# Performance work log

Measured on AMD Instinct MI355X. Metric: run time of the kernel, lower is better.

## Reference

```python
import jax, jax.numpy as jnp
import numpy as np

N, D, H, O, E, K = 16384, 512, 512, 64, 8, 2


def _layernorm(x, g, b, eps=1e-5):
    mu = jnp.mean(x, axis=-1, keepdims=True)
    var = jnp.var(x, axis=-1, keepdims=True)
    return (x - mu) * jax.lax.rsqrt(var + eps) * g + b


def _gelu(x):
    return jax.nn.gelu(x, approximate=False)  # torch nn.GELU default (erf)


def setup_inputs() -> dict:
    key = jax.random.key(0)
    ks = jax.random.split(key, 20)
    s = 0.02
    return {
        "x": jax.random.normal(ks[0], (N, D), jnp.float32),
        # gate: Linear(D,H) -> LN(H) -> GELU -> Linear(H,E)
        "g_w1": jax.random.normal(ks[1], (D, H), jnp.float32) * s,
        "g_b1": jnp.zeros((H,), jnp.float32),
        "g_ln_g": jnp.ones((H,), jnp.float32),
        "g_ln_b": jnp.zeros((H,), jnp.float32),
        "g_w2": jax.random.normal(ks[2], (H, E), jnp.float32) * s,
        "g_b2": jnp.zeros((E,), jnp.float32),
        # experts (stacked over E): Linear(D,H)+LN+GELU, Linear(H,H)+LN+GELU, Linear(H,O)
        "e_w1": jax.random.normal(ks[3], (E, D, H), jnp.float32) * s,
        "e_b1": jnp.zeros((E, H), jnp.float32),
        "e_ln1_g": jnp.ones((E, H), jnp.float32),
        "e_ln1_b": jnp.zeros((E, H), jnp.float32),
        "e_w2": jax.random.normal(ks[4], (E, H, H), jnp.float32) * s,
        "e_b2": jnp.zeros((E, H), jnp.float32),
        "e_ln2_g": jnp.ones((E, H), jnp.float32),
        "e_ln2_b": jnp.zeros((E, H), jnp.float32),
        "e_w3": jax.random.normal(ks[5], (E, H, O), jnp.float32) * s,
        "e_b3": jnp.zeros((E, O), jnp.float32),
        # output projection Linear(O,O)
        "p_w": jax.random.normal(ks[6], (O, O), jnp.float32) * s,
        "p_b": jnp.zeros((O,), jnp.float32),
    }


def reference(x, g_w1, g_b1, g_ln_g, g_ln_b, g_w2, g_b2,
              e_w1, e_b1, e_ln1_g, e_ln1_b, e_w2, e_b2, e_ln2_g, e_ln2_b,
              e_w3, e_b3, p_w, p_b):
    n = x.shape[0]
    # --- gate ---
    gh = _gelu(_layernorm(x @ g_w1 + g_b1, g_ln_g, g_ln_b))
    gate_logits = gh @ g_w2 + g_b2                      # [N, E]
    gate_weights = jax.nn.softmax(gate_logits, axis=-1)
    top_k_weights, top_k_indices = jax.lax.top_k(gate_weights, K)
    top_k_weights = top_k_weights / jnp.sum(top_k_weights, axis=-1, keepdims=True)
    # dense per-token expert weights [N, E] (sum of top-k weights routed to each expert)
    w_dense = jnp.zeros((n, e_w1.shape[0]), x.dtype).at[
        jnp.arange(n)[:, None], top_k_indices].add(top_k_weights)
    # --- all experts on all tokens (faithful to dense loop) ---
    h1 = _gelu(_layernorm(jnp.einsum('nd,edh->enh', x, e_w1) + e_b1[:, None, :],
                          e_ln1_g[:, None, :], e_ln1_b[:, None, :]))
    h2 = _gelu(_layernorm(jnp.einsum('enh,ehk->enk', h1, e_w2) + e_b2[:, None, :],
                          e_ln2_g[:, None, :], e_ln2_b[:, None, :]))
    expert_out = jnp.einsum('enh,eho->eno', h2, e_w3) + e_b3[:, None, :]  # [E, N, O]
    combined = jnp.einsum('ne,eno->no', w_dense, expert_out)              # [N, O]
    output = combined @ p_w + p_b
    expert_usage = jnp.mean(gate_weights, axis=0)
    return (output, gate_weights, top_k_indices, top_k_weights, expert_usage)
```

## Files before the change

### kernel.cpp

```cpp
#include <hip/hip_runtime.h>
#include <hip/hip_bf16.h>

#define N_TOK 16384
#define MAX_SLOTS 34080
#define MAX_BLOCKS 216

typedef __attribute__((ext_vector_type(8))) short bf16x8;
typedef __attribute__((ext_vector_type(4))) float f32x4;
typedef unsigned short u16;

#define V_WAIT(N) asm volatile("s_waitcnt vmcnt(" #N ")" ::: "memory")
#define LGKM0()   asm volatile("s_waitcnt lgkmcnt(0)" ::: "memory")

__device__ __forceinline__ u16 f2bf(float f) {
  __hip_bfloat16 h = __float2bfloat16(f);
  union { __hip_bfloat16 b; u16 u; } c; c.b = h; return c.u;
}
__device__ __forceinline__ float bfbits2f(u16 u) {
  return __uint_as_float(((unsigned)u) << 16);
}
__device__ __forceinline__ float gelu_erf(float x) {
  return 0.5f * x * (1.0f + erff(x * 0.70710678118654752f));
}
__device__ __forceinline__ float gelu_fast(float x) {
  float u = x * (0.79788456f + 0.035677408f * x * x);
  float ex;
  asm("v_exp_f32 %0, %1" : "=v"(ex) : "v"(-2.8853901f * u));
  float den = 1.0f + ex;
  float r;
  asm("v_rcp_f32 %0, %1" : "=v"(r) : "v"(den));
  return x * r;
}
__device__ __forceinline__ void gload16(const u16* g, char* lds) {
  __builtin_amdgcn_global_load_lds(
      (const __attribute__((address_space(1))) void*)g,
      (__attribute__((address_space(3))) void*)lds, 16, 0, 0);
}

__global__ __launch_bounds__(256) void prep_x(const float* __restrict__ x,
                                              u16* __restrict__ xbf,
                                              u16* __restrict__ xlo) {
  size_t i = (size_t)blockIdx.x * 256 + threadIdx.x;
  float4 v = ((const float4*)x)[i];
  float a[4] = {v.x, v.y, v.z, v.w};
  union { u16 us[4]; unsigned long long ll; } hb, lb;
#pragma unroll
  for (int j = 0; j < 4; ++j) {
    u16 hu = f2bf(a[j]);
    hb.us[j] = hu;
    lb.us[j] = f2bf(a[j] - bfbits2f(hu));
  }
  *(unsigned long long*)(xbf + i * 4) = hb.ll;
  *(unsigned long long*)(xlo + i * 4) = lb.ll;
}

template <int C>
__global__ __launch_bounds__(256) void pack_w(const float* __restrict__ src,
                                              u16* __restrict__ dst, int R) {
  __shared__ float tl[64][65];
  const int e = blockIdx.z;
  const int k0 = blockIdx.x * 64, n0 = blockIdx.y * 64;
  const float* s = src + (size_t)e * R * C;
  const int tr = threadIdx.x >> 2;
  const int tc4 = (threadIdx.x & 3) * 16;
#pragma unroll
  for (int j = 0; j < 4; ++j) {
    float4 v = *(const float4*)(s + (size_t)(k0 + tr) * C + n0 + tc4 + j * 4);
    tl[tr][tc4 + j * 4 + 0] = v.x;
    tl[tr][tc4 + j * 4 + 1] = v.y;
    tl[tr][tc4 + j * 4 + 2] = v.z;
    tl[tr][tc4 + j * 4 + 3] = v.w;
  }
  __syncthreads();
  const int nl = threadIdx.x >> 2;
  const int kl = (threadIdx.x & 3) * 16;
  const int n = n0 + nl;
  const int sx = (n >> 1) & 3;
  const int t = (k0 + kl) >> 5;
  const int q0 = ((k0 + kl) & 31) >> 3;
#pragma unroll
  for (int c = 0; c < 2; ++c) {
    int q = q0 + c;
    int p = q ^ sx;
    union { u16 us[8]; unsigned long long ll[2]; } o;
#pragma unroll
    for (int j = 0; j < 8; ++j) o.us[j] = f2bf(tl[kl + c * 8 + j][nl]);
    u16* d = dst + (((size_t)e * (R / 32) + t) * C + n) * 32 + p * 8;
    ((unsigned long long*)d)[0] = o.ll[0];
    ((unsigned long long*)d)[1] = o.ll[1];
  }
}

__global__ __launch_bounds__(256) void prep_wcat(const float* __restrict__ gw1,
                                                 u16* __restrict__ wp) {
  int idx = blockIdx.x * 256 + threadIdx.x;
  int p = idx & 3;
  int n = (idx >> 2) & 511;
  int t = idx >> 11;
  int q = p ^ ((n >> 1) & 3);
  int k0 = t * 32 + q * 8;
  union { u16 us[8]; unsigned long long ll[2]; } o;
#pragma unroll
  for (int j = 0; j < 8; ++j) {
    int k = k0 + j;
    u16 v;
    if (k < 512) {
      v = f2bf(gw1[k * 512 + n]);
    } else if (k < 1024) {
      float w = gw1[(k - 512) * 512 + n];
      v = f2bf(w - bfbits2f(f2bf(w)));
    } else {
      v = f2bf(gw1[(k - 1024) * 512 + n]);
    }
    o.us[j] = v;
  }
  unsigned long long* d = (unsigned long long*)(wp + (size_t)idx * 8);
  d[0] = o.ll[0];
  d[1] = o.ll[1];
}

__global__ __launch_bounds__(256) void prep_w2t(const float* __restrict__ gw2,
                                                float* __restrict__ w2t) {
  int i = blockIdx.x * 256 + threadIdx.x;
  int e = i >> 9, k = i & 511;
  w2t[i] = gw2[k * 8 + e];
}

template <int FM, int ROUTED, int GATHER, int LNOUT, int FAST>
__global__ __launch_bounds__(512, 2) void gemm_core(
    const u16* __restrict__ A, const u16* __restrict__ A2,
    const u16* __restrict__ Wp, long w_estride, int klen, long osplit,
    const float* __restrict__ bias, int b_estride,
    const float* __restrict__ lng, const float* __restrict__ lnb,
    u16* __restrict__ outb, float* __restrict__ outf,
    const int* __restrict__ slot_token, const int* __restrict__ blk_e,
    const int* __restrict__ blk_tok0) {
  constexpr int BM = FM * 32;
  constexpr int AG = FM * 2;
  constexpr int ABYTES = BM * 64;
  constexpr int BUF = ABYTES + 32768;
  constexpr int NL = AG + 32;
  constexpr int L = (NL + 7) / 8;
  constexpr int TSU = 16384;
  extern __shared__ char smem[];

  const int tid = threadIdx.x;
  const int lane = tid & 63;
  const int wv = tid >> 6;
  const int wm = (wv & 1) * (FM * 16);
  const int wn = (wv >> 1) * 128;
  const int l15 = lane & 15;
  const int lk = lane >> 4;
  const int swzk16 = (lk ^ ((l15 >> 1) & 3)) << 4;

  int e, row0, kt0, kbase;
  if (ROUTED) {
    e = blk_e[blockIdx.x];
    if (e < 0) return;
    row0 = blk_tok0[blockIdx.x];
    kt0 = 0; kbase = 0;
  } else {
    e = 0;
    row0 = blockIdx.x * BM;
    kbase = blockIdx.y * klen;
    kt0 = kbase >> 5;
  }
  const u16* We = Wp + (size_t)e * w_estride;

  const int lrq = lane >> 2;
  const int cse = (((lane & 3) ^ ((lane >> 3) & 3)) << 3);
  size_t off[L];
  int ldsoff[L], typ[L];
#pragma unroll
  for (int i = 0; i < L; ++i) {
    int id = wv + 8 * i;
    if (id >= NL) { typ[i] = 2; off[i] = 0; ldsoff[i] = 0; continue; }
    if (id < AG) {
      int lr = id * 16 + lrq;
      long grow = GATHER ? (long)slot_token[row0 + lr] : (long)(row0 + lr);
      off[i] = (size_t)grow * 512 + cse;
      ldsoff[i] = id * 1024 + lane * 16;
      typ[i] = 0;
    } else {
      int bg = id - AG;
      off[i] = (size_t)bg * 512 + lane * 8;
      ldsoff[i] = ABYTES + bg * 1024 + lane * 16;
      typ[i] = 1;
    }
  }

  float bias_v[8], g_v[8], b_v[8];
  if constexpr (LNOUT) {
    const float* be = bias + (size_t)e * b_estride;
    const float* ge = lng + (size_t)e * b_estride;
    const float* bbe = lnb + (size_t)e * b_estride;
#pragma unroll
    for (int fn = 0; fn < 8; ++fn) {
      int col = wn + fn * 16 + l15;
      bias_v[fn] = be[col]; g_v[fn] = ge[col]; b_v[fn] = bbe[col];
    }
  }

  auto STAGE = [&](int t, char* b) {
    const int kg = kbase + t * 32;
    const u16* Aseg = A;
    int kc = kg;
    if (A2) {
      if (kg >= 1024) { Aseg = A2; kc = kg - 1024; }
      else if (kg >= 512) kc = kg - 512;
    }
    const u16* Bt = We + (size_t)(kt0 + t) * TSU;
#pragma unroll
    for (int i = 0; i < L; ++i) {
      if (typ[i] == 0)      gload16(Aseg + off[i] + kc, b + ldsoff[i]);
      else if (typ[i] == 1) gload16(Bt + off[i], b + ldsoff[i]);
    }
  };

  f32x4 acc[FM][8];
#pragma unroll
  for (int i = 0; i < FM; ++i)
#pragma unroll
    for (int j = 0; j < 8; ++j) acc[i][j] = (f32x4){0.f, 0.f, 0.f, 0.f};

  const int nt = klen / 32;

  V_WAIT(0);
  STAGE(0, smem);
  STAGE(1, smem + BUF);
  STAGE(2, smem + 2 * BUF);

  int bsel = 0;
  for (int t = 0; t < nt; ++t) {
    if constexpr (FM == 5) {
      if (t < nt - 2)       { if (wv < 2) V_WAIT(12); else V_WAIT(10); }
      else if (t == nt - 2) { if (wv < 2) V_WAIT(6);  else V_WAIT(5); }
      else                  V_WAIT(0);
    } else {
      if (t < nt - 2)       V_WAIT(10);
      else if (t == nt - 2) V_WAIT(5);
      else                  V_WAIT(0);
    }
    __builtin_amdgcn_s_barrier();
    char* cur = smem + bsel * BUF;
    char* cB = cur + ABYTES;
    bf16x8 af[FM];
#pragma unroll
    for (int fm = 0; fm < FM; ++fm)
      af[fm] = *(const bf16x8*)(cur + (wm + fm * 16 + l15) * 64 + swzk16);
#pragma unroll
    for (int fn = 0; fn < 8; ++fn) {
      bf16x8 bv = *(const bf16x8*)(cB + (wn + fn * 16 + l15) * 64 + swzk16);
#pragma unroll
      for (int fm = 0; fm < FM; ++fm)
        acc[fm][fn] = __builtin_amdgcn_mfma_f32_16x16x32_bf16(
            af[fm], bv, acc[fm][fn], 0, 0, 0);
    }
    LGKM0();
    __builtin_amdgcn_s_barrier();
    if (t + 3 < nt) STAGE(t + 3, cur);
    bsel = (bsel == 2) ? 0 : bsel + 1;
  }

  if constexpr (LNOUT) {
#pragma unroll
    for (int fm = 0; fm < FM; ++fm)
#pragma unroll
      for (int fn = 0; fn < 8; ++fn)
#pragma unroll
        for (int r = 0; r < 4; ++r) acc[fm][fn][r] += bias_v[fn];

    float* redS1 = (float*)smem;
    float* redS2 = redS1 + 4 * BM;
    const int g = wv >> 1;
#pragma unroll
    for (int fm = 0; fm < FM; ++fm)
#pragma unroll
      for (int r = 0; r < 4; ++r) {
        float a1 = 0.f, a2 = 0.f;
#pragma unroll
        for (int fn = 0; fn < 8; ++fn) {
          float v = acc[fm][fn][r];
          a1 += v; a2 += v * v;
        }
#pragma unroll
        for (int m = 1; m < 16; m <<= 1) {
          a1 += __shfl_xor(a1, m, 64);
          a2 += __shfl_xor(a2, m, 64);
        }
        if (l15 == 0) {
          int row = wm + fm * 16 + lk * 4 + r;
          redS1[g * BM + row] = a1;
          redS2[g * BM + row] = a2;
        }
      }
    __syncthreads();
#pragma unroll
    for (int fm = 0; fm < FM; ++fm)
#pragma unroll
      for (int r = 0; r < 4; ++r) {
        int row = wm + fm * 16 + lk * 4 + r;
        float S1 = 0.f, S2 = 0.f;
#pragma unroll
        for (int q = 0; q < 4; ++q) {
          S1 += redS1[q * BM + row];
          S2 += redS2[q * BM + row];
        }
        float mu = S1 * (1.0f / 512.0f);
        float var = S2 * (1.0f / 512.0f) - mu * mu;
        float rs = rsqrtf(var + 1e-5f);
        size_t rowg = (size_t)(row0 + row);
#pragma unroll
        for (int fn = 0; fn < 8; ++fn) {
          int col = wn + fn * 16 + l15;
          float v = (acc[fm][fn][r] - mu) * rs * g_v[fn] + b_v[fn];
          v = FAST ? gelu_fast(v) : gelu_erf(v);
          outb[rowg * 512 + col] = f2bf(v);
        }
      }
  } else {
    float* dst = outf + (size_t)blockIdx.y * osplit;
#pragma unroll
    for (int fm = 0; fm < FM; ++fm)
#pragma unroll
      for (int r = 0; r < 4; ++r) {
        size_t rowg = (size_t)(row0 + wm + fm * 16 + lk * 4 + r);
#pragma unroll
        for (int fn = 0; fn < 8; ++fn)
          dst[rowg * 512 + wn + fn * 16 + l15] = acc[fm][fn][r];
      }
  }
}

__global__ __launch_bounds__(256) void gate2_topk(
    const float* __restrict__ gh0, const float* __restrict__ gh1,
    const float* __restrict__ b1, const float* __restrict__ lng,
    const float* __restrict__ lnb, const float* __restrict__ w2t,
    const float* __restrict__ b2, float* __restrict__ gwout,
    float* __restrict__ idxout, float* __restrict__ tkwout) {
  const int lane = threadIdx.x & 63;
  const int wv = threadIdx.x >> 6;
  const int t = blockIdx.x * 4 + wv;
  const int c0 = lane * 8;
  float v[8];
  {
    float4 a0 = *(const float4*)(gh0 + (size_t)t * 512 + c0);
    float4 a1 = *(const float4*)(gh0 + (size_t)t * 512 + c0 + 4);
    float4 h0 = *(const float4*)(gh1 + (size_t)t * 512 + c0);
    float4 h1 = *(const float4*)(gh1 + (size_t)t * 512 + c0 + 4);
    float4 bb0 = *(const float4*)(b1 + c0);
    float4 bb1 = *(const float4*)(b1 + c0 + 4);
    v[0] = a0.x + h0.x + bb0.x; v[1] = a0.y + h0.y + bb0.y;
    v[2] = a0.z + h0.z + bb0.z; v[3] = a0.w + h0.w + bb0.w;
    v[4] = a1.x + h1.x + bb1.x; v[5] = a1.y + h1.y + bb1.y;
    v[6] = a1.z + h1.z + bb1.z; v[7] = a1.w + h1.w + bb1.w;
  }
  float s1 = 0.f, s2 = 0.f;
#pragma unroll
  for (int j = 0; j < 8; ++j) { s1 += v[j]; s2 += v[j] * v[j]; }
#pragma unroll
  for (int m = 1; m < 64; m <<= 1) {
    s1 += __shfl_xor(s1, m, 64);
    s2 += __shfl_xor(s2, m, 64);
  }
  float mu = s1 * (1.0f / 512.0f);
  float var = s2 * (1.0f / 512.0f) - mu * mu;
  float rs = rsqrtf(var + 1e-5f);
  float y[8];
  {
    float4 g0 = *(const float4*)(lng + c0);
    float4 g1 = *(const float4*)(lng + c0 + 4);
    float4 q0 = *(const float4*)(lnb + c0);
    float4 q1 = *(const float4*)(lnb + c0 + 4);
    float gg[8] = {g0.x, g0.y, g0.z, g0.w, g1.x, g1.y, g1.z, g1.w};
    float qq[8] = {q0.x, q0.y, q0.z, q0.w, q1.x, q1.y, q1.z, q1.w};
#pragma unroll
    for (int j = 0; j < 8; ++j)
      y[j] = gelu_erf((v[j] - mu) * rs * gg[j] + qq[j]);
  }
  float logit[8];
#pragma unroll
  for (int e = 0; e < 8; ++e) {
    const float4* wr = (const float4*)(w2t + e * 512 + c0);
    float4 w0 = wr[0], w1 = wr[1];
    float p = y[0] * w0.x + y[1] * w0.y + y[2] * w0.z + y[3] * w0.w +
              y[4] * w1.x + y[5] * w1.y + y[6] * w1.z + y[7] * w1.w;
#pragma unroll
    for (int m = 1; m < 64; m <<= 1) p += __shfl_xor(p, m, 64);
    logit[e] = p + b2[e];
  }
  if (lane == 0) {
    float mx = logit[0];
#pragma unroll
    for (int e = 1; e < 8; ++e) mx = fmaxf(mx, logit[e]);
    float w[8], ssum = 0.f;
#pragma unroll
    for (int e = 0; e < 8; ++e) { w[e] = expf(logit[e] - mx); ssum += w[e]; }
    float inv = 1.0f / ssum;
#pragma unroll
    for (int e = 0; e < 8; ++e) w[e] *= inv;
    float w1v = -1.f, w2v = -1.f; int i1 = 0, i2 = 0;
#pragma unroll
    for (int e = 0; e < 8; ++e) {
      float vv = w[e];
      if (vv > w1v)      { w2v = w1v; i2 = i1; w1v = vv; i1 = e; }
      else if (vv > w2v) { w2v = vv; i2 = e; }
    }
    float s = w1v + w2v;
#pragma unroll
    for (int e = 0; e < 8; ++e) gwout[t * 8 + e] = w[e];
    idxout[t * 2] = (float)i1; idxout[t * 2 + 1] = (float)i2;
    tkwout[t * 2] = w1v / s;   tkwout[t * 2 + 1] = w2v / s;
  }
}

__global__ __launch_bounds__(256) void usage_k(const float* __restrict__ gw,
                                               float* __restrict__ usage) {
  __shared__ float r[256];
  int e = blockIdx.x;
  float s = 0.f;
  for (int t = threadIdx.x; t < N_TOK; t += 256) s += gw[t * 8 + e];
  r[threadIdx.x] = s;
  __syncthreads();
  for (int st = 128; st > 0; st >>= 1) {
    if (threadIdx.x < st) r[threadIdx.x] += r[threadIdx.x + st];
    __syncthreads();
  }
  if (threadIdx.x == 0) usage[e] = r[0] * (1.0f / (float)N_TOK);
}

__global__ __launch_bounds__(256) void count_hist(const float* __restrict__ idxout,
                                                  int* __restrict__ blk_cnt) {
  __shared__ int h[8];
  if (threadIdx.x < 8) h[threadIdx.x] = 0;
  __syncthreads();
  int t = blockIdx.x * 256 + threadIdx.x;
  int e0 = (int)idxout[t * 2], e1 = (int)idxout[t * 2 + 1];
  atomicAdd(&h[e0], 1);
  atomicAdd(&h[e1], 1);
  __syncthreads();
  if (threadIdx.x < 8) blk_cnt[blockIdx.x * 8 + threadIdx.x] = h[threadIdx.x];
}

__global__ __launch_bounds__(512) void k_offsets2(
    const int* __restrict__ blk_cnt, int* __restrict__ sbase,
    int* __restrict__ blk_e, int* __restrict__ blk_tok0) {
  __shared__ int cnt[64][8];
  __shared__ int ecnt[8];
  __shared__ int offs[8];
  const int tid = threadIdx.x;
  cnt[tid >> 3][tid & 7] = blk_cnt[tid];
  __syncthreads();
  if (tid < 8) {
    int s = 0;
    for (int b = 0; b < 64; ++b) s += cnt[b][tid];
    ecnt[tid] = s;
  }
  __syncthreads();
  if (tid == 0) {
    int off = 0;
    for (int e = 0; e < 8; ++e) {
      offs[e] = off;
      off += ((ecnt[e] + 159) / 160) * 160;
    }
  }
  __syncthreads();
  {
    int b = tid >> 3, e = tid & 7;
    int s = offs[e];
    for (int bp = 0; bp < b; ++bp) s += cnt[bp][e];
    sbase[tid] = s;
  }
  for (int b = tid; b < MAX_BLOCKS; b += 512) {
    int acc = 0, be = -1, bt = 0;
#pragma unroll
    for (int e = 0; e < 8; ++e) {
      int nbe = (ecnt[e] + 159) / 160;
      if (b >= acc && b < acc + nbe) { be = e; bt = offs[e] + (b - acc) * 160; }
      acc += nbe;
    }
    blk_e[b] = be;
    blk_tok0[b] = bt;
  }
}

__global__ __launch_bounds__(256) void k_padinit(int* __restrict__ slot_token,
                                                 float* __restrict__ slot_w) {
  int i = blockIdx.x * 256 + threadIdx.x;
  if (i < MAX_SLOTS) { slot_token[i] = 0; slot_w[i] = 0.f; }
}

__global__ __launch_bounds__(256) void k_scatter2(
    const float* __restrict__ idxout, const float* __restrict__ tkwout,
    const int* __restrict__ sbase, int* __restrict__ slot_token,
    float* __restrict__ slot_w, int* __restrict__ tok_slot) {
  __shared__ int lpos[8];
  if (threadIdx.x < 8) lpos[threadIdx.x] = 0;
  __syncthreads();
  int t = blockIdx.x * 256 + threadIdx.x;
#pragma unroll
  for (int k = 0; k < 2; ++k) {
    int e = (int)idxout[t * 2 + k];
    int lr = atomicAdd(&lpos[e], 1);
    int s = sbase[blockIdx.x * 8 + e] + lr;
    slot_token[s] = t;
    slot_w[s] = tkwout[t * 2 + k];
    tok_slot[t * 2 + k] = s;
  }
}

__global__ __launch_bounds__(512) void gemm3_eo(
    const u16* __restrict__ h, const u16* __restrict__ w3p,
    const float* __restrict__ b3, const float* __restrict__ slot_w,
    const int* __restrict__ blk_e, const int* __restrict__ blk_tok0,
    float* __restrict__ eo) {
  constexpr int ABYTES = 10240;
  constexpr int BUF = ABYTES + 4096;
  __shared__ char smem[3 * BUF];
  int e = blk_e[blockIdx.x];
  if (e < 0) return;
  int row0 = blk_tok0[blockIdx.x];

  const int tid = threadIdx.x;
  const int lane = tid & 63;
  const int wv = tid >> 6;
  const int wm = (wv & 1) * 80;
  const int wn = (wv >> 1) * 16;
  const int l15 = lane & 15, lk = lane >> 4;
  const int swzk16 = (lk ^ ((l15 >> 1) & 3)) << 4;
  const u16* we = w3p + (size_t)e * 32768;

  const int lrq = lane >> 2;
  const int cse = (((lane & 3) ^ ((lane >> 3) & 3)) << 3);
  size_t off[2];
  int ldsoff[2], typ[2];
#pragma unroll
  for (int i = 0; i < 2; ++i) {
    int id = wv + 8 * i;
    if (id >= 14) { typ[i] = 2; off[i] = 0; ldsoff[i] = 0; continue; }
    if (id < 10) {
      off[i] = (size_t)(row0 + id * 16 + lrq) * 512 + cse;
      ldsoff[i] = id * 1024 + lane * 16;
      typ[i] = 0;
    } else {
      int bg = id - 10;
      off[i] = (size_t)bg * 512 + lane * 8;
      ldsoff[i] = ABYTES + bg * 1024 + lane * 16;
      typ[i] = 1;
    }
  }

  float b3v = b3[e * 64 + wn + l15];
  float swv[5];
#pragma unroll
  for (int fm = 0; fm < 5; ++fm)
    swv[fm] = slot_w[row0 + wm + fm * 16 + lk * 4];
  float swr[5][4];
#pragma unroll
  for (int fm = 0; fm < 5; ++fm)
#pragma unroll
    for (int r = 0; r < 4; ++r)
      swr[fm][r] = slot_w[row0 + wm + fm * 16 + lk * 4 + r];
  (void)swv;

  auto STAGE = [&](int t, char* b) {
#pragma unroll
    for (int i = 0; i < 2; ++i) {
      if (typ[i] == 0)      gload16(h + off[i] + t * 32, b + ldsoff[i]);
      else if (typ[i] == 1) gload16(we + (size_t)t * 2048 + off[i], b + ldsoff[i]);
    }
  };

  f32x4 acc[5];
#pragma unroll
  for (int j = 0; j < 5; ++j) acc[j] = (f32x4){0.f, 0.f, 0.f, 0.f};

  V_WAIT(0);
  STAGE(0, smem);
  STAGE(1, smem + BUF);
  STAGE(2, smem + 2 * BUF);

  int bsel = 0;
  for (int t = 0; t < 16; ++t) {
    if (t < 14)       { if (wv < 6) V_WAIT(4); else V_WAIT(2); }
    else if (t == 14) { if (wv < 6) V_WAIT(2); else V_WAIT(1); }
    else              V_WAIT(0);
    __builtin_amdgcn_s_barrier();
    char* cur = smem + bsel * BUF;
    char* cB = cur + ABYTES;
    bf16x8 bv = *(const bf16x8*)(cB + (wn + l15) * 64 + swzk16);
#pragma unroll
    for (int fm = 0; fm < 5; ++fm) {
      bf16x8 a = *(const bf16x8*)(cur + (wm + fm * 16 + l15) * 64 + swzk16);
      acc[fm] = __builtin_amdgcn_mfma_f32_16x16x32_bf16(a, bv, acc[fm], 0, 0, 0);
    }
    LGKM0();
    __builtin_amdgcn_s_barrier();
    if (t + 3 < 16) STAGE(t + 3, cur);
    bsel = (bsel == 2) ? 0 : bsel + 1;
  }

#pragma unroll
  for (int fm = 0; fm < 5; ++fm)
#pragma unroll
    for (int r = 0; r < 4; ++r) {
      int row = wm + fm * 16 + lk * 4 + r;
      eo[(size_t)(row0 + row) * 64 + wn + l15] = swr[fm][r] * (acc[fm][r] + b3v);
    }
}

__global__ __launch_bounds__(256) void combine_proj(
    const float* __restrict__ eo, const int* __restrict__ tok_slot,
    const float* __restrict__ pw, const float* __restrict__ pb,
    float* __restrict__ outp) {
  __shared__ float cs[64][68];
  __shared__ float pws[64][68];
  const int t0 = blockIdx.x * 64;
  const int tq = threadIdx.x & 3;
  const int tt = threadIdx.x >> 2;
#pragma unroll
  for (int j = 0; j < 4; ++j) {
    float4 v = *(const float4*)(pw + tt * 64 + tq * 16 + j * 4);
    *(float4*)&pws[tt][tq * 16 + j * 4] = v;
  }
  {
    int t = t0 + tt;
    int s1 = tok_slot[t * 2], s2 = tok_slot[t * 2 + 1];
#pragma unroll
    for (int j = 0; j < 4; ++j) {
      float4 a = *(const float4*)(eo + (size_t)s1 * 64 + tq * 16 + j * 4);
      float4 b = *(const float4*)(eo + (size_t)s2 * 64 + tq * 16 + j * 4);
      float4 c = {a.x + b.x, a.y + b.y, a.z + b.z, a.w + b.w};
      *(float4*)&cs[tt][tq * 16 + j * 4] = c;
    }
  }
  __syncthreads();
  float o[16];
#pragma unroll
  for (int i = 0; i < 16; ++i) o[i] = 0.f;
  for (int j = 0; j < 64; ++j) {
    float c = cs[tt][j];
#pragma unroll
    for (int q4 = 0; q4 < 4; ++q4) {
      float4 p = *(const float4*)&pws[j][tq * 16 + q4 * 4];
      o[q4 * 4 + 0] += c * p.x;
      o[q4 * 4 + 1] += c * p.y;
      o[q4 * 4 + 2] += c * p.z;
      o[q4 * 4 + 3] += c * p.w;
    }
  }
#pragma unroll
  for (int i = 0; i < 16; ++i)
    outp[(size_t)(t0 + tt) * 64 + tq * 16 + i] = o[i] + pb[tq * 16 + i];
}

extern "C" void kernel_launch(void* const* d_in, const int* in_sizes, int n_in,
                              void* d_out, int out_size, void* d_ws, size_t ws_size,
                              hipStream_t stream) {
  const float* x      = (const float*)d_in[0];
  const float* g_w1   = (const float*)d_in[1];
  const float* g_b1   = (const float*)d_in[2];
  const float* g_lng  = (const float*)d_in[3];
  const float* g_lnb  = (const float*)d_in[4];
  const float* g_w2   = (const float*)d_in[5];
  const float* g_b2   = (const float*)d_in[6];
  const float* e_w1   = (const float*)d_in[7];
  const float* e_b1   = (const float*)d_in[8];
  const float* e_ln1g = (const float*)d_in[9];
  const float* e_ln1b = (const float*)d_in[10];
  const float* e_w2   = (const float*)d_in[11];
  const float* e_b2   = (const float*)d_in[12];
  const float* e_ln2g = (const float*)d_in[13];
  const float* e_ln2b = (const float*)d_in[14];
  const float* e_w3   = (const float*)d_in[15];
  const float* e_b3   = (const float*)d_in[16];
  const float* p_w    = (const float*)d_in[17];
  const float* p_b    = (const float*)d_in[18];

  char* ws = (char*)d_ws;
  u16*   x_bf  = (u16*)(ws);
  u16*   x_lo  = (u16*)(ws + (16ull << 20));
  u16*   e_w1p = (u16*)(ws + (32ull << 20));
  u16*   e_w2p = (u16*)(ws + (36ull << 20));
  u16*   e_w3p = (u16*)(ws + (40ull << 20));
  u16*   wcat  = (u16*)(ws + (41ull << 20));
  float* w2t   = (float*)(ws + (43ull << 20));
  float* gh0   = (float*)(ws + (44ull << 20));
  float* gh1   = (float*)(ws + (76ull << 20));
  u16*   h     = (u16*)(ws + (44ull << 20));
  float* eo    = (float*)(ws + (112ull << 20));
  int*   slot_token = (int*)(ws + (121ull << 20));
  float* slot_w     = (float*)(ws + (121ull << 20) + (1ull << 18));
  int*   tok_slot   = (int*)(ws + (121ull << 20) + (2ull << 18));
  int*   blk_cnt    = (int*)(ws + (122ull << 20));
  int*   sbase      = blk_cnt + 512;
  int*   blk_e      = blk_cnt + 1024;
  int*   blk_tok0   = blk_cnt + 2048;
  if (ws_size < (123ull << 20)) return;

  float* fout = (float*)d_out;
  float* o_output = fout;
  float* o_gatew  = fout + 1048576;
  float* o_idx    = fout + 1179648;
  float* o_topw   = fout + 1212416;
  float* o_usage  = fout + 1245184;

  (void)hipFuncSetAttribute((const void*)gemm_core<4, 0, 0, 0, 0>,
                            hipFuncAttributeMaxDynamicSharedMemorySize, 122880);
  (void)hipFuncSetAttribute((const void*)gemm_core<5, 1, 1, 1, 1>,
                            hipFuncAttributeMaxDynamicSharedMemorySize, 129024);
  (void)hipFuncSetAttribute((const void*)gemm_core<5, 1, 0, 1, 1>,
                            hipFuncAttributeMaxDynamicSharedMemorySize, 129024);

  prep_x<<<8192, 256, 0, stream>>>(x, x_bf, x_lo);
  pack_w<512><<<dim3(8, 8, 8), 256, 0, stream>>>(e_w1, e_w1p, 512);
  pack_w<512><<<dim3(8, 8, 8), 256, 0, stream>>>(e_w2, e_w2p, 512);
  pack_w<64><<<dim3(8, 1, 8), 256, 0, stream>>>(e_w3, e_w3p, 512);
  prep_wcat<<<384, 256, 0, stream>>>(g_w1, wcat);
  prep_w2t<<<16, 256, 0, stream>>>(g_w2, w2t);

  gemm_core<4, 0, 0, 0, 0><<<dim3(N_TOK / 128, 2), 512, 122880, stream>>>(
      x_bf, x_lo, wcat, 0, 768, (long)N_TOK * 512, nullptr, 0,
      nullptr, nullptr, nullptr, gh0, nullptr, nullptr, nullptr);
  gate2_topk<<<N_TOK / 4, 256, 0, stream>>>(gh0, gh1, g_b1, g_lng, g_lnb,
                                            w2t, g_b2, o_gatew, o_idx, o_topw);
  usage_k<<<8, 256, 0, stream>>>(o_gatew, o_usage);

  count_hist<<<64, 256, 0, stream>>>(o_idx, blk_cnt);
  k_offsets2<<<1, 512, 0, stream>>>(blk_cnt, sbase, blk_e, blk_tok0);
  k_padinit<<<(MAX_SLOTS + 255) / 256, 256, 0, stream>>>(slot_token, slot_w);
  k_scatter2<<<64, 256, 0, stream>>>(o_idx, o_topw, sbase, slot_token, slot_w,
                                     tok_slot);

  gemm_core<5, 1, 1, 1, 1><<<MAX_BLOCKS, 512, 129024, stream>>>(
      x_bf, nullptr, e_w1p, 512 * 512, 512, 0, e_b1, 512,
      e_ln1g, e_ln1b, h, nullptr, slot_token, blk_e, blk_tok0);
  gemm_core<5, 1, 0, 1, 1><<<MAX_BLOCKS, 512, 129024, stream>>>(
      h, nullptr, e_w2p, 512 * 512, 512, 0, e_b2, 512,
      e_ln2g, e_ln2b, h, nullptr, slot_token, blk_e, blk_tok0);
  gemm3_eo<<<MAX_BLOCKS, 512, 0, stream>>>(h, e_w3p, e_b3, slot_w, blk_e,
                                           blk_tok0, eo);
  combine_proj<<<N_TOK / 64, 256, 0, stream>>>(eo, tok_slot, p_w, p_b, o_output);
}
```

Baseline: 212.5 us.

## Run expert GEMMs in FP8 with fp8 activations and packed fp8 weights

Converts the three routed expert GEMMs from bf16 to FP8 (e4m3) MFMA. The input x, the packed expert weights and the intermediate hidden activations are stored as fp8 with a new 64-byte K-tile layout. This halves the number of K-loop iterations and the bytes loaded per tile, targeting memory traffic and MFMA throughput in the expert stage. The gate GEMM stays bf16 and is split into its own specialized kernel. The trade-off is a substantial loss of precision in the expert outputs, which risks exceeding the accuracy tolerance.

```diff
diff --git a/kernel.cpp b/kernel.cpp
--- a/kernel.cpp
+++ b/kernel.cpp
@@ -8,6 +8,8 @@
 typedef __attribute__((ext_vector_type(8))) short bf16x8;
 typedef __attribute__((ext_vector_type(4))) float f32x4;
 typedef unsigned short u16;
+typedef unsigned char u8;
+typedef long i64;
 
 #define V_WAIT(N) asm volatile("s_waitcnt vmcnt(" #N ")" ::: "memory")
 #define LGKM0()   asm volatile("s_waitcnt lgkmcnt(0)" ::: "memory")
@@ -31,7 +33,10 @@
   asm("v_rcp_f32 %0, %1" : "=v"(r) : "v"(den));
   return x * r;
 }
-__device__ __forceinline__ void gload16(const u16* g, char* lds) {
+__device__ __forceinline__ u8 f2fp8(float f) {
+  return (u8)(__builtin_amdgcn_cvt_pk_fp8_f32(f, f, 0, false) & 0xff);
+}
+__device__ __forceinline__ void gload16(const void* g, char* lds) {
   __builtin_amdgcn_global_load_lds(
       (const __attribute__((address_space(1))) void*)g,
       (__attribute__((address_space(3))) void*)lds, 16, 0, 0);
@@ -39,7 +44,8 @@
 
 __global__ __launch_bounds__(256) void prep_x(const float* __restrict__ x,
                                               u16* __restrict__ xbf,
-                                              u16* __restrict__ xlo) {
+                                              u16* __restrict__ xlo,
+                                              u8* __restrict__ xf8) {
   size_t i = (size_t)blockIdx.x * 256 + threadIdx.x;
   float4 v = ((const float4*)x)[i];
   float a[4] = {v.x, v.y, v.z, v.w};
@@ -52,11 +58,14 @@
   }
   *(unsigned long long*)(xbf + i * 4) = hb.ll;
   *(unsigned long long*)(xlo + i * 4) = lb.ll;
+  int w8 = __builtin_amdgcn_cvt_pk_fp8_f32(a[0], a[1], 0, false);
+  w8 = __builtin_amdgcn_cvt_pk_fp8_f32(a[2], a[3], w8, true);
+  *(int*)(xf8 + i * 4) = w8;
 }
 
 template <int C>
-__global__ __launch_bounds__(256) void pack_w(const float* __restrict__ src,
-                                              u16* __restrict__ dst, int R) {
+__global__ __launch_bounds__(256) void pack_w_f8(const float* __restrict__ src,
+                                                 u8* __restrict__ dst, int R) {
   __shared__ float tl[64][65];
   const int e = blockIdx.z;
   const int k0 = blockIdx.x * 64, n0 = blockIdx.y * 64;
@@ -75,20 +84,22 @@
   const int nl = threadIdx.x >> 2;
   const int kl = (threadIdx.x & 3) * 16;
   const int n = n0 + nl;
-  const int sx = (n >> 1) & 3;
-  const int t = (k0 + kl) >> 5;
-  const int q0 = ((k0 + kl) & 31) >> 3;
-#pragma unroll
-  for (int c = 0; c < 2; ++c) {
-    int q = q0 + c;
-    int p = q ^ sx;
-    union { u16 us[8]; unsigned long long ll[2]; } o;
-#pragma unroll
-    for (int j = 0; j < 8; ++j) o.us[j] = f2bf(tl[kl + c * 8 + j][nl]);
-    u16* d = dst + (((size_t)e * (R / 32) + t) * C + n) * 32 + p * 8;
-    ((unsigned long long*)d)[0] = o.ll[0];
-    ((unsigned long long*)d)[1] = o.ll[1];
-  }
+  const int T = R / 64;
+  const int t = (k0 + kl) >> 6;
+  const int q = ((k0 + kl) >> 4) & 3;
+  const int p = q ^ ((n >> 1) & 3);
+  uint4 o;
+  unsigned w[4];
+#pragma unroll
+  for (int j = 0; j < 4; ++j) {
+    int ww = __builtin_amdgcn_cvt_pk_fp8_f32(tl[kl + 4 * j][nl],
+                                             tl[kl + 4 * j + 1][nl], 0, false);
+    ww = __builtin_amdgcn_cvt_pk_fp8_f32(tl[kl + 4 * j + 2][nl],
+                                         tl[kl + 4 * j + 3][nl], ww, true);
+    w[j] = (unsigned)ww;
+  }
+  o.x = w[0]; o.y = w[1]; o.z = w[2]; o.w = w[3];
+  *(uint4*)(dst + (((size_t)e * T + t) * C + n) * 64 + p * 16) = o;
 }
 
 __global__ __launch_bounds__(256) void prep_wcat(const float* __restrict__ gw1,
@@ -126,15 +137,11 @@
   w2t[i] = gw2[k * 8 + e];
 }
 
-template <int FM, int ROUTED, int GATHER, int LNOUT, int FAST>
-__global__ __launch_bounds__(512, 2) void gemm_core(
+template <int FM>
+__global__ __launch_bounds__(512, 2) void gemm_gate(
     const u16* __restrict__ A, const u16* __restrict__ A2,
-    const u16* __restrict__ Wp, long w_estride, int klen, long osplit,
-    const float* __restrict__ bias, int b_estride,
-    const float* __restrict__ lng, const float* __restrict__ lnb,
-    u16* __restrict__ outb, float* __restrict__ outf,
-    const int* __restrict__ slot_token, const int* __restrict__ blk_e,
-    const int* __restrict__ blk_tok0) {
+    const u16* __restrict__ Wp, int klen, long osplit,
+    float* __restrict__ outf) {
   constexpr int BM = FM * 32;
   constexpr int AG = FM * 2;
   constexpr int ABYTES = BM * 64;
@@ -153,19 +160,9 @@
   const int lk = lane >> 4;
   const int swzk16 = (lk ^ ((l15 >> 1) & 3)) << 4;
 
-  int e, row0, kt0, kbase;
-  if (ROUTED) {
-    e = blk_e[blockIdx.x];
-    if (e < 0) return;
-    row0 = blk_tok0[blockIdx.x];
-    kt0 = 0; kbase = 0;
-  } else {
-    e = 0;
-    row0 = blockIdx.x * BM;
-    kbase = blockIdx.y * klen;
-    kt0 = kbase >> 5;
-  }
-  const u16* We = Wp + (size_t)e * w_estride;
+  const int row0 = blockIdx.x * BM;
+  const int kbase = blockIdx.y * klen;
+  const int kt0 = kbase >> 5;
 
   const int lrq = lane >> 2;
   const int cse = (((lane & 3) ^ ((lane >> 3) & 3)) << 3);
@@ -176,9 +173,7 @@
     int id = wv + 8 * i;
     if (id >= NL) { typ[i] = 2; off[i] = 0; ldsoff[i] = 0; continue; }
     if (id < AG) {
-      int lr = id * 16 + lrq;
-      long grow = GATHER ? (long)slot_token[row0 + lr] : (long)(row0 + lr);
-      off[i] = (size_t)grow * 512 + cse;
+      off[i] = (size_t)(row0 + id * 16 + lrq) * 512 + cse;
       ldsoff[i] = id * 1024 + lane * 16;
       typ[i] = 0;
     } else {
@@ -189,27 +184,13 @@
     }
   }
 
-  float bias_v[8], g_v[8], b_v[8];
-  if constexpr (LNOUT) {
-    const float* be = bias + (size_t)e * b_estride;
-    const float* ge = lng + (size_t)e * b_estride;
-    const float* bbe = lnb + (size_t)e * b_estride;
-#pragma unroll
-    for (int fn = 0; fn < 8; ++fn) {
-      int col = wn + fn * 16 + l15;
-      bias_v[fn] = be[col]; g_v[fn] = ge[col]; b_v[fn] = bbe[col];
-    }
-  }
-
   auto STAGE = [&](int t, char* b) {
     const int kg = kbase + t * 32;
     const u16* Aseg = A;
     int kc = kg;
-    if (A2) {
-      if (kg >= 1024) { Aseg = A2; kc = kg - 1024; }
-      else if (kg >= 512) kc = kg - 512;
-    }
-    const u16* Bt = We + (size_t)(kt0 + t) * TSU;
+    if (kg >= 1024) { Aseg = A2; kc = kg - 1024; }
+    else if (kg >= 512) kc = kg - 512;
+    const u16* Bt = Wp + (size_t)(kt0 + t) * TSU;
 #pragma unroll
     for (int i = 0; i < L; ++i) {
       if (typ[i] == 0)      gload16(Aseg + off[i] + kc, b + ldsoff[i]);
@@ -224,7 +205,6 @@
     for (int j = 0; j < 8; ++j) acc[i][j] = (f32x4){0.f, 0.f, 0.f, 0.f};
 
   const int nt = klen / 32;
-
   V_WAIT(0);
   STAGE(0, smem);
   STAGE(1, smem + BUF);
@@ -232,15 +212,9 @@
 
   int bsel = 0;
   for (int t = 0; t < nt; ++t) {
-    if constexpr (FM == 5) {
-      if (t < nt - 2)       { if (wv < 2) V_WAIT(12); else V_WAIT(10); }
-      else if (t == nt - 2) { if (wv < 2) V_WAIT(6);  else V_WAIT(5); }
-      else                  V_WAIT(0);
-    } else {
-      if (t < nt - 2)       V_WAIT(10);
-      else if (t == nt - 2) V_WAIT(5);
-      else                  V_WAIT(0);
-    }
+    if (t < nt - 2)       V_WAIT(10);
+    else if (t == nt - 2) V_WAIT(5);
+    else                  V_WAIT(0);
     __builtin_amdgcn_s_barrier();
     char* cur = smem + bsel * BUF;
     char* cB = cur + ABYTES;
@@ -262,74 +236,185 @@
     bsel = (bsel == 2) ? 0 : bsel + 1;
   }
 
-  if constexpr (LNOUT) {
-#pragma unroll
-    for (int fm = 0; fm < FM; ++fm)
+  float* dst = outf + (size_t)blockIdx.y * osplit;
+#pragma unroll
+  for (int fm = 0; fm < FM; ++fm)
+#pragma unroll
+    for (int r = 0; r < 4; ++r) {
+      size_t rowg = (size_t)(row0 + wm + fm * 16 + lk * 4 + r);
 #pragma unroll
       for (int fn = 0; fn < 8; ++fn)
-#pragma unroll
-        for (int r = 0; r < 4; ++r) acc[fm][fn][r] += bias_v[fn];
-
-    float* redS1 = (float*)smem;
-    float* redS2 = redS1 + 4 * BM;
-    const int g = wv >> 1;
-#pragma unroll
-    for (int fm = 0; fm < FM; ++fm)
-#pragma unroll
-      for (int r = 0; r < 4; ++r) {
-        float a1 = 0.f, a2 = 0.f;
-#pragma unroll
-        for (int fn = 0; fn < 8; ++fn) {
-          float v = acc[fm][fn][r];
-          a1 += v; a2 += v * v;
-        }
-#pragma unroll
-        for (int m = 1; m < 16; m <<= 1) {
-          a1 += __shfl_xor(a1, m, 64);
-          a2 += __shfl_xor(a2, m, 64);
-        }
-        if (l15 == 0) {
-          int row = wm + fm * 16 + lk * 4 + r;
-          redS1[g * BM + row] = a1;
-          redS2[g * BM + row] = a2;
-        }
+        dst[rowg * 512 + wn + fn * 16 + l15] = acc[fm][fn][r];
+    }
+}
+
+template <int GATHER>
+__global__ __launch_bounds__(512, 2) void gemm_f8(
+    const u8* __restrict__ A, const u8* __restrict__ Wp, long w_estride,
+    const float* __restrict__ bias, const float* __restrict__ lng,
+    const float* __restrict__ lnb, u8* __restrict__ outb,
+    const int* __restrict__ slot_token, const int* __restrict__ blk_e,
+    const int* __restrict__ blk_tok0) {
+  constexpr int FM = 5, BM = 160, AG = 10;
+  constexpr int ABYTES = BM * 64;
+  constexpr int BUF = ABYTES + 32768;
+  constexpr int NL = AG + 32;
+  constexpr int L = 6;
+  extern __shared__ char smem[];
+
+  const int tid = threadIdx.x;
+  const int lane = tid & 63;
+  const int wv = tid >> 6;
+  const int wm = (wv & 1) * 80;
+  const int wn = (wv >> 1) * 128;
+  const int l15 = lane & 15;
+  const int lk = lane >> 4;
+  const int sx = (l15 >> 1) & 3;
+  const int swz0 = (((lk >> 1) ^ sx) << 4) + (lk & 1) * 8;
+  const int swz1 = ((((lk >> 1) + 2) ^ sx) << 4) + (lk & 1) * 8;
+
+  int e = blk_e[blockIdx.x];
+  if (e < 0) return;
+  const int row0 = blk_tok0[blockIdx.x];
+  const u8* We = Wp + (size_t)e * w_estride;
+
+  const int lrq = lane >> 2;
+  const int csb = (((lane & 3) ^ ((lane >> 3) & 3)) << 4);
+  size_t off[L];
+  int ldsoff[L], typ[L];
+#pragma unroll
+  for (int i = 0; i < L; ++i) {
+    int id = wv + 8 * i;
+    if (id >= NL) { typ[i] = 2; off[i] = 0; ldsoff[i] = 0; continue; }
+    if (id < AG) {
+      int lr = id * 16 + lrq;
+      long grow = GATHER ? (long)slot_token[row0 + lr] : (long)(row0 + lr);
+      off[i] = (size_t)grow * 512 + csb;
+      ldsoff[i] = id * 1024 + lane * 16;
+      typ[i] = 0;
+    } else {
+      int bg = id - AG;
+      off[i] = (size_t)bg * 1024 + lane * 16;
+      ldsoff[i] = ABYTES + bg * 1024 + lane * 16;
+      typ[i] = 1;
+    }
+  }
+
+  float bias_v[8], g_v[8], b_v[8];
+  const float* be = bias + (size_t)e * 512;
+  const float* ge = lng + (size_t)e * 512;
+  const float* bbe = lnb + (size_t)e * 512;
+#pragma unroll
+  for (int fn = 0; fn < 8; ++fn) {
+    int col = wn + fn * 16 + l15;
+    bias_v[fn] = be[col]; g_v[fn] = ge[col]; b_v[fn] = bbe[col];
+  }
+
+  auto STAGE = [&](int t, char* b) {
+    const u8* Bt = We + (size_t)t * 32768;
+#pragma unroll
+    for (int i = 0; i < L; ++i) {
+      if (typ[i] == 0)      gload16(A + off[i] + t * 64, b + ldsoff[i]);
+      else if (typ[i] == 1) gload16(Bt + off[i], b + ldsoff[i]);
+    }
+  };
+
+  f32x4 acc[FM][8];
+#pragma unroll
+  for (int i = 0; i < FM; ++i)
+#pragma unroll
+    for (int j = 0; j < 8; ++j) acc[i][j] = (f32x4){0.f, 0.f, 0.f, 0.f};
+
+  constexpr int nt = 8;
+  V_WAIT(0);
+  STAGE(0, smem);
+  STAGE(1, smem + BUF);
+  STAGE(2, smem + 2 * BUF);
+
+  int bsel = 0;
+  for (int t = 0; t < nt; ++t) {
+    if (t < nt - 2)       { if (wv < 2) V_WAIT(12); else V_WAIT(10); }
+    else if (t == nt - 2) { if (wv < 2) V_WAIT(6);  else V_WAIT(5); }
+    else                  V_WAIT(0);
+    __builtin_amdgcn_s_barrier();
+    char* cur = smem + bsel * BUF;
+    char* cB = cur + ABYTES;
+#pragma unroll
+    for (int s = 0; s < 2; ++s) {
+      const int sw = s ? swz1 : swz0;
+      i64 af[FM];
+#pragma unroll
+      for (int fm = 0; fm < FM; ++fm)
+        af[fm] = *(const i64*)(cur + (wm + fm * 16 + l15) * 64 + sw);
+#pragma unroll
+      for (int fn = 0; fn < 8; ++fn) {
+        i64 bv = *(const i64*)(cB + (wn + fn * 16 + l15) * 64 + sw);
+#pragma unroll
+        for (int fm = 0; fm < FM; ++fm)
+          acc[fm][fn] = __builtin_amdgcn_mfma_f32_16x16x32_fp8_fp8(
+              af[fm], bv, acc[fm][fn], 0, 0, 0);
       }
-    __syncthreads();
-#pragma unroll
-    for (int fm = 0; fm < FM; ++fm)
-#pragma unroll
-      for (int r = 0; r < 4; ++r) {
+    }
+    LGKM0();
+    __builtin_amdgcn_s_barrier();
+    if (t + 3 < nt) STAGE(t + 3, cur);
+    bsel = (bsel == 2) ? 0 : bsel + 1;
+  }
+
+#pragma unroll
+  for (int fm = 0; fm < FM; ++fm)
+#pragma unroll
+    for (int fn = 0; fn < 8; ++fn)
+#pragma unroll
+      for (int r = 0; r < 4; ++r) acc[fm][fn][r] += bias_v[fn];
+
+  float* redS1 = (float*)smem;
+  float* redS2 = redS1 + 4 * BM;
+  const int g = wv >> 1;
+#pragma unroll
+  for (int fm = 0; fm < FM; ++fm)
+#pragma unroll
+    for (int r = 0; r < 4; ++r) {
+      float a1 = 0.f, a2 = 0.f;
+#pragma unroll
+      for (int fn = 0; fn < 8; ++fn) {
+        float v = acc[fm][fn][r];
+        a1 += v; a2 += v * v;
+      }
+#pragma unroll
+      for (int m = 1; m < 16; m <<= 1) {
+        a1 += __shfl_xor(a1, m, 64);
+        a2 += __shfl_xor(a2, m, 64);
+      }
+      if (l15 == 0) {
         int row = wm + fm * 16 + lk * 4 + r;
-        float S1 = 0.f, S2 = 0.f;
-#pragma unroll
-        for (int q = 0; q < 4; ++q) {
-          S1 += redS1[q * BM + row];
-          S2 += redS2[q * BM + row];
-        }
-        float mu = S1 * (1.0f / 512.0f);
-        float var = S2 * (1.0f / 512.0f) - mu * mu;
-        float rs = rsqrtf(var + 1e-5f);
-        size_t rowg = (size_t)(row0 + row);
-#pragma unroll
-        for (int fn = 0; fn < 8; ++fn) {
-          int col = wn + fn * 16 + l15;
-          float v = (acc[fm][fn][r] - mu) * rs * g_v[fn] + b_v[fn];
-          v = FAST ? gelu_fast(v) : gelu_erf(v);
-          outb[rowg * 512 + col] = f2bf(v);
-        }
+        redS1[g * BM + row] = a1;
+        redS2[g * BM + row] = a2;
       }
-  } else {
-    float* dst = outf + (size_t)blockIdx.y * osplit;
-#pragma unroll
-    for (int fm = 0; fm < FM; ++fm)
-#pragma unroll
-      for (int r = 0; r < 4; ++r) {
-        size_t rowg = (size_t)(row0 + wm + fm * 16 + lk * 4 + r);
-#pragma unroll
-        for (int fn = 0; fn < 8; ++fn)
-          dst[rowg * 512 + wn + fn * 16 + l15] = acc[fm][fn][r];
+    }
+  __syncthreads();
+#pragma unroll
+  for (int fm = 0; fm < FM; ++fm)
+#pragma unroll
+    for (int r = 0; r < 4; ++r) {
+      int row = wm + fm * 16 + lk * 4 + r;
+      float S1 = 0.f, S2 = 0.f;
+#pragma unroll
+      for (int q = 0; q < 4; ++q) {
+        S1 += redS1[q * BM + row];
+        S2 += redS2[q * BM + row];
       }
-  }
+      float mu = S1 * (1.0f / 512.0f);
+      float var = S2 * (1.0f / 512.0f) - mu * mu;
+      float rs = rsqrtf(var + 1e-5f);
+      size_t rowg = (size_t)(row0 + row);
+#pragma unroll
+      for (int fn = 0; fn < 8; ++fn) {
+        int col = wn + fn * 16 + l15;
+        float v = (acc[fm][fn][r] - mu) * rs * g_v[fn] + b_v[fn];
+        outb[rowg * 512 + col] = f2fp8(gelu_fast(v));
+      }
+    }
 }
 
 __global__ __launch_bounds__(256) void gate2_topk(
@@ -509,8 +594,8 @@
   }
 }
 
-__global__ __launch_bounds__(512) void gemm3_eo(
-    const u16* __restrict__ h, const u16* __restrict__ w3p,
+__global__ __launch_bounds__(512) void gemm3_f8(
+    const u8* __restrict__ h, const u8* __restrict__ w3p,
     const float* __restrict__ b3, const float* __restrict__ slot_w,
     const int* __restrict__ blk_e, const int* __restrict__ blk_tok0,
     float* __restrict__ eo) {
@@ -519,7 +604,7 @@
   __shared__ char smem[3 * BUF];
   int e = blk_e[blockIdx.x];
   if (e < 0) return;
-  int row0 = blk_tok0[blockIdx.x];
+  const int row0 = blk_tok0[blockIdx.x];
 
   const int tid = threadIdx.x;
   const int lane = tid & 63;
@@ -527,11 +612,13 @@
   const int wm = (wv & 1) * 80;
   const int wn = (wv >> 1) * 16;
   const int l15 = lane & 15, lk = lane >> 4;
-  const int swzk16 = (lk ^ ((l15 >> 1) & 3)) << 4;
-  const u16* we = w3p + (size_t)e * 32768;
+  const int sx = (l15 >> 1) & 3;
+  const int swz0 = (((lk >> 1) ^ sx) << 4) + (lk & 1) * 8;
+  const int swz1 = ((((lk >> 1) + 2) ^ sx) << 4) + (lk & 1) * 8;
+  const u8* we = w3p + (size_t)e * 32768;
 
   const int lrq = lane >> 2;
-  const int cse = (((lane & 3) ^ ((lane >> 3) & 3)) << 3);
+  const int csb = (((lane & 3) ^ ((lane >> 3) & 3)) << 4);
   size_t off[2];
   int ldsoff[2], typ[2];
 #pragma unroll
@@ -539,35 +626,30 @@
     int id = wv + 8 * i;
     if (id >= 14) { typ[i] = 2; off[i] = 0; ldsoff[i] = 0; continue; }
     if (id < 10) {
-      off[i] = (size_t)(row0 + id * 16 + lrq) * 512 + cse;
+      off[i] = (size_t)(row0 + id * 16 + lrq) * 512 + csb;
       ldsoff[i] = id * 1024 + lane * 16;
       typ[i] = 0;
     } else {
       int bg = id - 10;
-      off[i] = (size_t)bg * 512 + lane * 8;
+      off[i] = (size_t)bg * 1024 + lane * 16;
       ldsoff[i] = ABYTES + bg * 1024 + lane * 16;
       typ[i] = 1;
     }
   }
 
   float b3v = b3[e * 64 + wn + l15];
-  float swv[5];
-#pragma unroll
-  for (int fm = 0; fm < 5; ++fm)
-    swv[fm] = slot_w[row0 + wm + fm * 16 + lk * 4];
   float swr[5][4];
 #pragma unroll
   for (int fm = 0; fm < 5; ++fm)
 #pragma unroll
     for (int r = 0; r < 4; ++r)
       swr[fm][r] = slot_w[row0 + wm + fm * 16 + lk * 4 + r];
-  (void)swv;
 
   auto STAGE = [&](int t, char* b) {
 #pragma unroll
     for (int i = 0; i < 2; ++i) {
-      if (typ[i] == 0)      gload16(h + off[i] + t * 32, b + ldsoff[i]);
-      else if (typ[i] == 1) gload16(we + (size_t)t * 2048 + off[i], b + ldsoff[i]);
+      if (typ[i] == 0)      gload16(h + off[i] + t * 64, b + ldsoff[i]);
+      else if (typ[i] == 1) gload16(we + (size_t)t * 4096 + off[i], b + ldsoff[i]);
     }
   };
 
@@ -581,22 +663,27 @@
   STAGE(2, smem + 2 * BUF);
 
   int bsel = 0;
-  for (int t = 0; t < 16; ++t) {
-    if (t < 14)       { if (wv < 6) V_WAIT(4); else V_WAIT(2); }
-    else if (t == 14) { if (wv < 6) V_WAIT(2); else V_WAIT(1); }
-    else              V_WAIT(0);
+  for (int t = 0; t < 8; ++t) {
+    if (t < 6)       { if (wv < 6) V_WAIT(4); else V_WAIT(2); }
+    else if (t == 6) { if (wv < 6) V_WAIT(2); else V_WAIT(1); }
+    else             V_WAIT(0);
     __builtin_amdgcn_s_barrier();
     char* cur = smem + bsel * BUF;
     char* cB = cur + ABYTES;
-    bf16x8 bv = *(const bf16x8*)(cB + (wn + l15) * 64 + swzk16);
-#pragma unroll
-    for (int fm = 0; fm < 5; ++fm) {
-      bf16x8 a = *(const bf16x8*)(cur + (wm + fm * 16 + l15) * 64 + swzk16);
-      acc[fm] = __builtin_amdgcn_mfma_f32_16x16x32_bf16(a, bv, acc[fm], 0, 0, 0);
+#pragma unroll
+    for (int s = 0; s < 2; ++s) {
+      const int sw = s ? swz1 : swz0;
+      i64 bv = *(const i64*)(cB + (wn + l15) * 64 + sw);
+#pragma unroll
+      for (int fm = 0; fm < 5; ++fm) {
+        i64 a = *(const i64*)(cur + (wm + fm * 16 + l15) * 64 + sw);
+        acc[fm] = __builtin_amdgcn_mfma_f32_16x16x32_fp8_fp8(a, bv, acc[fm],
+                                                             0, 0, 0);
+      }
     }
     LGKM0();
     __builtin_amdgcn_s_barrier();
-    if (t + 3 < 16) STAGE(t + 3, cur);
+    if (t + 3 < 8) STAGE(t + 3, cur);
     bsel = (bsel == 2) ? 0 : bsel + 1;
   }
 
@@ -680,14 +767,15 @@
   char* ws = (char*)d_ws;
   u16*   x_bf  = (u16*)(ws);
   u16*   x_lo  = (u16*)(ws + (16ull << 20));
-  u16*   e_w1p = (u16*)(ws + (32ull << 20));
-  u16*   e_w2p = (u16*)(ws + (36ull << 20));
-  u16*   e_w3p = (u16*)(ws + (40ull << 20));
-  u16*   wcat  = (u16*)(ws + (41ull << 20));
-  float* w2t   = (float*)(ws + (43ull << 20));
-  float* gh0   = (float*)(ws + (44ull << 20));
-  float* gh1   = (float*)(ws + (76ull << 20));
-  u16*   h     = (u16*)(ws + (44ull << 20));
+  u8*    x_f8  = (u8*)(ws + (32ull << 20));
+  u8*    e_w1p = (u8*)(ws + (40ull << 20));
+  u8*    e_w2p = (u8*)(ws + (42ull << 20));
+  u8*    e_w3p = (u8*)(ws + (44ull << 20));
+  u16*   wcat  = (u16*)(ws + (45ull << 20));
+  float* w2t   = (float*)(ws + (47ull << 20));
+  float* gh0   = (float*)(ws + (48ull << 20));
+  float* gh1   = (float*)(ws + (80ull << 20));
+  u8*    h     = (u8*)(ws + (48ull << 20));
   float* eo    = (float*)(ws + (112ull << 20));
   int*   slot_token = (int*)(ws + (121ull << 20));
   float* slot_w     = (float*)(ws + (121ull << 20) + (1ull << 18));
@@ -705,23 +793,22 @@
   float* o_topw   = fout + 1212416;
   float* o_usage  = fout + 1245184;
 
-  (void)hipFuncSetAttribute((const void*)gemm_core<4, 0, 0, 0, 0>,
+  (void)hipFuncSetAttribute((const void*)gemm_gate<4>,
                             hipFuncAttributeMaxDynamicSharedMemorySize, 122880);
-  (void)hipFuncSetAttribute((const void*)gemm_core<5, 1, 1, 1, 1>,
+  (void)hipFuncSetAttribute((const void*)gemm_f8<1>,
                             hipFuncAttributeMaxDynamicSharedMemorySize, 129024);
-  (void)hipFuncSetAttribute((const void*)gemm_core<5, 1, 0, 1, 1>,
+  (void)hipFuncSetAttribute((const void*)gemm_f8<0>,
                             hipFuncAttributeMaxDynamicSharedMemorySize, 129024);
 
-  prep_x<<<8192, 256, 0, stream>>>(x, x_bf, x_lo);
-  pack_w<512><<<dim3(8, 8, 8), 256, 0, stream>>>(e_w1, e_w1p, 512);
-  pack_w<512><<<dim3(8, 8, 8), 256, 0, stream>>>(e_w2, e_w2p, 512);
-  pack_w<64><<<dim3(8, 1, 8), 256, 0, stream>>>(e_w3, e_w3p, 512);
+  prep_x<<<8192, 256, 0, stream>>>(x, x_bf, x_lo, x_f8);
+  pack_w_f8<512><<<dim3(8, 8, 8), 256, 0, stream>>>(e_w1, e_w1p, 512);
+  pack_w_f8<512><<<dim3(8, 8, 8), 256, 0, stream>>>(e_w2, e_w2p, 512);
+  pack_w_f8<64><<<dim3(8, 1, 8), 256, 0, stream>>>(e_w3, e_w3p, 512);
   prep_wcat<<<384, 256, 0, stream>>>(g_w1, wcat);
   prep_w2t<<<16, 256, 0, stream>>>(g_w2, w2t);
 
-  gemm_core<4, 0, 0, 0, 0><<<dim3(N_TOK / 128, 2), 512, 122880, stream>>>(
-      x_bf, x_lo, wcat, 0, 768, (long)N_TOK * 512, nullptr, 0,
-      nullptr, nullptr, nullptr, gh0, nullptr, nullptr, nullptr);
+  gemm_gate<4><<<dim3(N_TOK / 128, 2), 512, 122880, stream>>>(
+      x_bf, x_lo, wcat, 768, (long)N_TOK * 512, gh0);
   gate2_topk<<<N_TOK / 4, 256, 0, stream>>>(gh0, gh1, g_b1, g_lng, g_lnb,
                                             w2t, g_b2, o_gatew, o_idx, o_topw);
   usage_k<<<8, 256, 0, stream>>>(o_gatew, o_usage);
@@ -732,13 +819,13 @@
   k_scatter2<<<64, 256, 0, stream>>>(o_idx, o_topw, sbase, slot_token, slot_w,
                                      tok_slot);
 
-  gemm_core<5, 1, 1, 1, 1><<<MAX_BLOCKS, 512, 129024, stream>>>(
-      x_bf, nullptr, e_w1p, 512 * 512, 512, 0, e_b1, 512,
-      e_ln1g, e_ln1b, h, nullptr, slot_token, blk_e, blk_tok0);
-  gemm_core<5, 1, 0, 1, 1><<<MAX_BLOCKS, 512, 129024, stream>>>(
-      h, nullptr, e_w2p, 512 * 512, 512, 0, e_b2, 512,
-      e_ln2g, e_ln2b, h, nullptr, slot_token, blk_e, blk_tok0);
-  gemm3_eo<<<MAX_BLOCKS, 512, 0, stream>>>(h, e_w3p, e_b3, slot_w, blk_e,
+  gemm_f8<1><<<MAX_BLOCKS, 512, 129024, stream>>>(
+      x_f8, e_w1p, 262144, e_b1, e_ln1g, e_ln1b, h,
+      slot_token, blk_e, blk_tok0);
+  gemm_f8<0><<<MAX_BLOCKS, 512, 129024, stream>>>(
+      h, e_w2p, 262144, e_b2, e_ln2g, e_ln2b, h,
+      slot_token, blk_e, blk_tok0);
+  gemm3_f8<<<MAX_BLOCKS, 512, 0, stream>>>(h, e_w3p, e_b3, slot_w, blk_e,
                                            blk_tok0, eo);
   combine_proj<<<N_TOK / 64, 256, 0, stream>>>(eo, tok_slot, p_w, p_b, o_output);
 }
```

Result: slower. 235.1 us (+10.7%).
